# Performance work log

Measured on AMD Instinct MI355X. Metric: run time of the kernel, lower is better.

The kernel has to match this reference:

```python
import jax, jax.numpy as jnp
import numpy as np

B, S, D, H, T = 64, 512, 768, 384, 22  # batch, seq, bert dim, lstm hidden, tagset+2


def setup_inputs() -> dict:
    key = jax.random.key(0)
    ks = jax.random.split(key, 14)
    hidden_states = jax.random.normal(ks[0], (B, S, D), jnp.float32)
    # strictly increasing wordpiece start offsets, -1 padded (per-sample variable length)
    nw = np.array([S // 2 - (b % 16) * 4 for b in range(B)])  # number of valid start ids
    sid = -np.ones((B, S), np.int64)
    msk = np.zeros((B, S), np.int64)
    for b in range(B):
        sid[b, : nw[b]] = 1 + 2 * np.arange(nw[b])  # max = 2*nw-1 <= S-1
        msk[b, : nw[b] + 1] = 1  # word-level mask: nw+1 words incl. CLS slot
    start_ids = jnp.asarray(sid)
    masks = jnp.asarray(msk)
    sc = 0.05
    h0 = jax.random.normal(ks[1], (2, B, H), jnp.float32)
    c0 = jax.random.normal(ks[2], (2, B, H), jnp.float32)
    W_ih_f = jax.random.normal(ks[3], (4 * H, D), jnp.float32) * sc
    W_hh_f = jax.random.normal(ks[4], (4 * H, H), jnp.float32) * sc
    b_ih_f = jax.random.normal(ks[5], (4 * H,), jnp.float32) * sc
    b_hh_f = jax.random.normal(ks[6], (4 * H,), jnp.float32) * sc
    W_ih_b = jax.random.normal(ks[7], (4 * H, D), jnp.float32) * sc
    W_hh_b = jax.random.normal(ks[8], (4 * H, H), jnp.float32) * sc
    b_ih_b = jax.random.normal(ks[9], (4 * H,), jnp.float32) * sc
    b_hh_b = jax.random.normal(ks[10], (4 * H,), jnp.float32) * sc
    W_lin = jax.random.normal(ks[11], (T, 2 * H), jnp.float32) * sc
    b_lin = jax.random.normal(ks[12], (T,), jnp.float32) * sc
    return {"hidden_states": hidden_states, "h0": h0, "c0": c0,
            "W_ih_f": W_ih_f, "W_hh_f": W_hh_f, "b_ih_f": b_ih_f, "b_hh_f": b_hh_f,
            "W_ih_b": W_ih_b, "W_hh_b": W_hh_b, "b_ih_b": b_ih_b, "b_hh_b": b_hh_b,
            "W_lin": W_lin, "b_lin": b_lin, "start_ids": start_ids, "masks": masks}


def _lstm_dir(x, h0, c0, Wih, Whh, bih, bhh, reverse):
    # x: [B,S,D]; torch gate order i,f,g,o
    xg = jnp.einsum('bsd,gd->bsg', x, Wih) + bih + bhh  # [B,S,4H]
    xs = jnp.swapaxes(xg, 0, 1)  # [S,B,4H]
    if reverse:
        xs = xs[::-1]

    def step(carry, xt):
        h, c = carry
        g = xt + h @ Whh.T
        i, f, gg, o = jnp.split(g, 4, axis=-1)
        c = jax.nn.sigmoid(f) * c + jax.nn.sigmoid(i) * jnp.tanh(gg)
        h = jax.nn.sigmoid(o) * jnp.tanh(c)
        return (h, c), h

    _, hs = jax.lax.scan(step, (h0, c0), xs)
    if reverse:
        hs = hs[::-1]
    return jnp.swapaxes(hs, 0, 1)  # [B,S,H]


def _align(hidden_states, start_ids, masks):
    # word t embedding: t==0 -> token 0 (CLS); 1<=t<n -> token start_ids[t]-1
    # (last wordpiece of word t); t==n -> token start_ids[n-1]; else zero-pad.
    Bb, Ss, _ = hidden_states.shape
    t = jnp.arange(Ss)[None, :]
    valid = start_ids >= 0
    n = valid.sum(-1)  # [B] number of valid start ids
    last_sid = jnp.take_along_axis(start_ids, (n - 1)[:, None], axis=1)  # [B,1]
    idx = jnp.where(t == 0, 0,
          jnp.where(t < n[:, None], start_ids - 1,
          jnp.where(t == n[:, None], last_sid, 0)))
    idx = jnp.clip(idx, 0, Ss - 1)
    gathered = jnp.take_along_axis(hidden_states, idx[:, :, None], axis=1)
    sent_len = masks.sum(-1)  # word-level lengths (second loop in torch code)
    keep = (t < sent_len[:, None])[:, :, None]
    return jnp.where(keep, gathered, 0.0)


def reference(hidden_states, h0, c0, W_ih_f, W_hh_f, b_ih_f, b_hh_f,
              W_ih_b, W_hh_b, b_ih_b, b_hh_b, W_lin, b_lin, start_ids, masks):
    embeds = _align(hidden_states, start_ids, masks)  # q=1,k=0 => wordpiece-only
    hf = _lstm_dir(embeds, h0[0], c0[0], W_ih_f, W_hh_f, b_ih_f, b_hh_f, False)
    hb = _lstm_dir(embeds, h0[1], c0[1], W_ih_b, W_hh_b, b_ih_b, b_hh_b, True)
    lstm_out = jnp.concatenate([hf, hb], axis=-1)  # [B,S,2H]
    # dropout1 is identity in eval mode
    feats = lstm_out @ W_lin.T + b_lin  # [B,S,T]
    return feats
```

## Files before the change

kernel.cpp:

```cpp
#include <hip/hip_runtime.h>

typedef unsigned short u16;
typedef unsigned int u32;
typedef unsigned long long u64;

typedef short bf16x8 __attribute__((ext_vector_type(8)));
typedef float f32x4 __attribute__((ext_vector_type(4)));
typedef u32 u32x4 __attribute__((ext_vector_type(4)));

#define NB 64
#define NS 512
#define ND 768
#define NH 384
#define NT_OUT 22
#define S2 272
#define NG 1536
#define MGEMM (NB*S2)
#define MAGIC 0x5A5AA5A5u
#define MAX_RETRY 1000000

__device__ __forceinline__ u16 f2b(float f) {
    u32 u = __float_as_uint(f);
    u32 r = (u + 0x7fffu + ((u >> 16) & 1u)) >> 16;
    return (u16)r;
}
__device__ __forceinline__ float b2f(u16 s) { return __uint_as_float(((u32)s) << 16); }

__device__ __forceinline__ float sigm(float x) {
    return __builtin_amdgcn_rcpf(1.f + __expf(-x));
}
__device__ __forceinline__ float tanh_(float x) {
    return 1.f - 2.f * __builtin_amdgcn_rcpf(1.f + __expf(2.f * x));
}

__device__ __forceinline__ void gl_lds16(const void* g, void* l) {
    __builtin_amdgcn_global_load_lds(
        (const __attribute__((address_space(1))) unsigned int*)g,
        (__attribute__((address_space(3))) unsigned int*)l, 16, 0, 0);
}

__device__ __forceinline__ u32 ld_sc0(const int* p) {
    u32 v;
    asm volatile("global_load_dword %0, %1, off sc0 nt\n\t"
                 "s_waitcnt vmcnt(0)"
                 : "=&v"(v) : "v"(p) : "memory");
    return v;
}
__device__ __forceinline__ void st_sc0(int* p, u32 v) {
    asm volatile("global_store_dword %0, %1, off sc0" :: "v"(p), "v"(v) : "memory");
}

__device__ __forceinline__ void ld6_fast_nw(const u32* p,
        u32x4& A, u32x4& B, u32x4& C, u32x4& D, u32x4& E, u32x4& F) {
    asm volatile(
        "global_load_dwordx4 %0, %6, off sc0 nt\n\t"
        "global_load_dwordx4 %1, %6, off offset:16 sc0 nt\n\t"
        "global_load_dwordx4 %2, %6, off offset:128 sc0 nt\n\t"
        "global_load_dwordx4 %3, %6, off offset:144 sc0 nt\n\t"
        "global_load_dwordx4 %4, %6, off offset:256 sc0 nt\n\t"
        "global_load_dwordx4 %5, %6, off offset:272 sc0 nt"
        : "=&v"(A), "=&v"(B), "=&v"(C), "=&v"(D), "=&v"(E), "=&v"(F)
        : "v"(p) : "memory");
}
__device__ __forceinline__ void ld6_fast_wt(const u32* p,
        u32x4& A, u32x4& B, u32x4& C, u32x4& D, u32x4& E, u32x4& F) {
    asm volatile(
        "global_load_dwordx4 %0, %6, off sc0 nt\n\t"
        "global_load_dwordx4 %1, %6, off offset:16 sc0 nt\n\t"
        "global_load_dwordx4 %2, %6, off offset:128 sc0 nt\n\t"
        "global_load_dwordx4 %3, %6, off offset:144 sc0 nt\n\t"
        "global_load_dwordx4 %4, %6, off offset:256 sc0 nt\n\t"
        "global_load_dwordx4 %5, %6, off offset:272 sc0 nt\n\t"
        "s_waitcnt vmcnt(0)"
        : "=&v"(A), "=&v"(B), "=&v"(C), "=&v"(D), "=&v"(E), "=&v"(F)
        : "v"(p) : "memory");
}
__device__ __forceinline__ void ld6_slow(const u32* p,
        u32x4& A, u32x4& B, u32x4& C, u32x4& D, u32x4& E, u32x4& F) {
    #pragma unroll
    for (int e = 0; e < 4; e++) {
        A[e] = __hip_atomic_load(p + e,      __ATOMIC_RELAXED, __HIP_MEMORY_SCOPE_AGENT);
        B[e] = __hip_atomic_load(p + 4 + e,  __ATOMIC_RELAXED, __HIP_MEMORY_SCOPE_AGENT);
        C[e] = __hip_atomic_load(p + 32 + e, __ATOMIC_RELAXED, __HIP_MEMORY_SCOPE_AGENT);
        D[e] = __hip_atomic_load(p + 36 + e, __ATOMIC_RELAXED, __HIP_MEMORY_SCOPE_AGENT);
        E[e] = __hip_atomic_load(p + 64 + e, __ATOMIC_RELAXED, __HIP_MEMORY_SCOPE_AGENT);
        F[e] = __hip_atomic_load(p + 68 + e, __ATOMIC_RELAXED, __HIP_MEMORY_SCOPE_AGENT);
    }
}
__device__ __forceinline__ void ld6_nw(bool fast, const u32* p,
        u32x4& A, u32x4& B, u32x4& C, u32x4& D, u32x4& E, u32x4& F) {
    if (fast) ld6_fast_nw(p, A, B, C, D, E, F);
    else      ld6_slow(p, A, B, C, D, E, F);
}
__device__ __forceinline__ void ld6_wt(bool fast, const u32* p,
        u32x4& A, u32x4& B, u32x4& C, u32x4& D, u32x4& E, u32x4& F) {
    if (fast) ld6_fast_wt(p, A, B, C, D, E, F);
    else      ld6_slow(p, A, B, C, D, E, F);
}
__device__ __forceinline__ void st8(bool fast, u32* p, u32x4 lo, u32x4 hi) {
    if (fast)
        asm volatile("global_store_dwordx4 %0, %1, off sc0\n\t"
                     "global_store_dwordx4 %0, %2, off offset:16 sc0"
                     :: "v"(p), "v"(lo), "v"(hi) : "memory");
    else {
        #pragma unroll
        for (int e = 0; e < 4; e++) {
            __hip_atomic_store(p + e,     lo[e], __ATOMIC_RELAXED, __HIP_MEMORY_SCOPE_AGENT);
            __hip_atomic_store(p + 4 + e, hi[e], __ATOMIC_RELAXED, __HIP_MEMORY_SCOPE_AGENT);
        }
    }
}
#define WAIT_VM(N) do { __builtin_amdgcn_sched_barrier(0); \
    asm volatile("s_waitcnt vmcnt(" #N ")" ::: "memory"); \
    __builtin_amdgcn_sched_barrier(0); } while (0)
__device__ __forceinline__ void ldsbar() {
    asm volatile("s_waitcnt lgkmcnt(0)" ::: "memory");
    __builtin_amdgcn_s_barrier();
    __builtin_amdgcn_sched_barrier(0);
}

__device__ __forceinline__ u32 sum6(const u32x4& a, const u32x4& b, const u32x4& c,
                                    const u32x4& d, const u32x4& e, const u32x4& f) {
    u32 s = (a[0] & 0xffffu) + (a[1] & 0xffffu) + (a[2] & 0xffffu) + (a[3] & 0xffffu);
    s += (b[0] & 0xffffu) + (b[1] & 0xffffu) + (b[2] & 0xffffu) + (b[3] & 0xffffu);
    s += (c[0] & 0xffffu) + (c[1] & 0xffffu) + (c[2] & 0xffffu) + (c[3] & 0xffffu);
    s += (d[0] & 0xffffu) + (d[1] & 0xffffu) + (d[2] & 0xffffu) + (d[3] & 0xffffu);
    s += (e[0] & 0xffffu) + (e[1] & 0xffffu) + (e[2] & 0xffffu) + (e[3] & 0xffffu);
    s += (f[0] & 0xffffu) + (f[1] & 0xffffu) + (f[2] & 0xffffu) + (f[3] & 0xffffu);
    return s;
}
__device__ __forceinline__ bf16x8 packf(const u32x4& lo, const u32x4& hi) {
    union { u32 q[4]; bf16x8 v; } U;
    U.q[0] = __builtin_amdgcn_perm(lo[1], lo[0], 0x07060302u);
    U.q[1] = __builtin_amdgcn_perm(lo[3], lo[2], 0x07060302u);
    U.q[2] = __builtin_amdgcn_perm(hi[1], hi[0], 0x07060302u);
    U.q[3] = __builtin_amdgcn_perm(hi[3], hi[2], 0x07060302u);
    return U.v;
}

__global__ void k_prep(const float* __restrict__ hidden, const int* __restrict__ start_ids,
                       const int* __restrict__ masks, u16* __restrict__ embeds) {
    int b = blockIdx.x >> 2;
    int quarter = blockIdx.x & 3;
    int tid = threadIdx.x;
    __shared__ int red[256];
    int cn = 0, cm = 0;
    for (int s = tid; s < NS; s += 256) {
        cn += (start_ids[b * NS + s] >= 0) ? 1 : 0;
        cm += (masks[b * NS + s] != 0) ? 1 : 0;
    }
    red[tid] = cn + (cm << 16);
    __syncthreads();
    #pragma unroll
    for (int off = 128; off > 0; off >>= 1) {
        if (tid < off) red[tid] += red[tid + off];
        __syncthreads();
    }
    int n = red[0] & 0xffff;
    int slen = red[0] >> 16;
    n = min(max(n, 1), NS);
    int last = start_ids[b * NS + n - 1];
    for (int t = quarter * 68; t < quarter * 68 + 68; ++t) {
        int idx;
        if (t == 0) idx = 0;
        else if (t < n) idx = start_ids[b * NS + t] - 1;
        else if (t == n) idx = last;
        else idx = 0;
        idx = min(max(idx, 0), NS - 1);
        bool keep = t < slen;
        const float* src = hidden + ((size_t)b * NS + idx) * ND;
        u16* dst = embeds + ((size_t)b * S2 + t) * ND;
        if (tid < 192) {
            float4 v = keep ? *(const float4*)(src + tid * 4) : make_float4(0.f, 0.f, 0.f, 0.f);
            union { u16 u[4]; uint2 q; } pk;
            pk.u[0] = f2b(v.x); pk.u[1] = f2b(v.y); pk.u[2] = f2b(v.z); pk.u[3] = f2b(v.w);
            *(uint2*)(dst + tid * 4) = pk.q;
        }
    }
}

__global__ void k_weights(const float* __restrict__ wf, const float* __restrict__ wb,
                          const float* __restrict__ bihf, const float* __restrict__ bhhf,
                          const float* __restrict__ bihb, const float* __restrict__ bhhb,
                          const float* __restrict__ h0,
                          u16* __restrict__ wihcat, float* __restrict__ biascat,
                          u16* __restrict__ h0buf) {
    int i0 = blockIdx.x * blockDim.x + threadIdx.x;
    int NTH = gridDim.x * blockDim.x;
    for (size_t i = i0; i < (size_t)2 * NG * ND; i += NTH) {
        size_t nrow = i / ND, k = i - nrow * ND;
        float v = (nrow < NG) ? wf[nrow * ND + k] : wb[(nrow - NG) * ND + k];
        wihcat[i] = f2b(v);
    }
    for (int i = i0; i < 2 * NG; i += NTH)
        biascat[i] = (i < NG) ? bihf[i] + bhhf[i] : bihb[i - NG] + bhhb[i - NG];
    for (int i = i0; i < 2 * NB * NH; i += NTH) h0buf[i] = f2b(h0[i]);
}

__global__ void k_packwhh(const float* __restrict__ whhf, const float* __restrict__ whhb,
                          u16* __restrict__ pack) {
    int ft = blockIdx.x * 256 + threadIdx.x;
    if (ft >= 2 * 4 * 4 * 6 * 12 * 64) return;
    int lane = ft & 63;
    int grp = ft >> 6;
    int ks = grp % 12; grp /= 12;
    int nt = grp % 6;  grp /= 6;
    int w  = grp & 3;  grp >>= 2;
    int qc = grp & 3;
    int d  = grp >> 2;
    const float* W = d ? whhb : whhf;
    int col = w * NH + qc * 96 + nt * 16 + (lane & 15);
    int k0 = ks * 32 + (lane >> 4) * 8;
    u16* dst = pack + (size_t)ft * 8;
    #pragma unroll
    for (int e = 0; e < 8; e++) dst[e] = f2b(W[(size_t)col * NH + k0 + e]);
}

__launch_bounds__(256, 2)
__global__ void k_gemm(const u16* __restrict__ A, const u16* __restrict__ Bw,
                       const float* __restrict__ biascat, u16* __restrict__ xg) {
    __shared__ u16 As[128 * 32];
    __shared__ u16 Bs[128 * 32];
    int tid = threadIdx.x;
    int lane = tid & 63, wid = tid >> 6;
    int l15 = lane & 15, q4 = lane >> 4;
    int bn = blockIdx.x;
    int bm = blockIdx.y;
    int wm = (wid >> 1) * 64, wn = (wid & 1) * 64;
    f32x4 acc[4][4] = {};
    for (int k0 = 0; k0 < ND; k0 += 32) {
        #pragma unroll
        for (int j = 0; j < 2; j++) {
            int fl = tid + j * 256;
            int row = fl >> 2, cb = fl & 3;
            const u16* ga = A + (size_t)(bm * 128 + row) * ND + k0 + cb * 8;
            gl_lds16(ga, &As[(size_t)(wid * 64 + j * 256) * 8]);
            const u16* gb = Bw + (size_t)(bn * 128 + row) * ND + k0 + cb * 8;
            gl_lds16(gb, &Bs[(size_t)(wid * 64 + j * 256) * 8]);
        }
        __syncthreads();
        bf16x8 af[4], bf[4];
        #pragma unroll
        for (int mt = 0; mt < 4; mt++)
            af[mt] = *(const bf16x8*)&As[(wm + mt * 16 + l15) * 32 + q4 * 8];
        #pragma unroll
        for (int nt = 0; nt < 4; nt++)
            bf[nt] = *(const bf16x8*)&Bs[(wn + nt * 16 + l15) * 32 + q4 * 8];
        #pragma unroll
        for (int mt = 0; mt < 4; mt++)
            #pragma unroll
            for (int nt = 0; nt < 4; nt++)
                acc[mt][nt] = __builtin_amdgcn_mfma_f32_16x16x32_bf16(af[mt], bf[nt], acc[mt][nt], 0, 0, 0);
        __syncthreads();
    }
    #pragma unroll
    for (int nt = 0; nt < 4; nt++) {
        int gn = bn * 128 + wn + nt * 16 + l15;
        int d = gn >= NG ? 1 : 0;
        int col = gn - d * NG;
        float bias = biascat[gn];
        #pragma unroll
        for (int mt = 0; mt < 4; mt++) {
            #pragma unroll
            for (int r = 0; r < 4; r++) {
                int m = bm * 128 + wm + mt * 16 + q4 * 4 + r;
                int b = m / S2, t = m - b * S2;
                float v = acc[mt][nt][r] + bias;
                xg[((size_t)(d * NB + b) * S2 + t) * NG + col] = f2b(v);
            }
        }
    }
}

__launch_bounds__(256, 1)
__global__ void k_recur(const u16* __restrict__ whhpack, const u16* __restrict__ xg,
                        const float* __restrict__ biascat, const u16* __restrict__ h0buf,
                        const float* __restrict__ c0, u16* __restrict__ hout,
                        int* __restrict__ flags, u32* __restrict__ xch) {
    const int blk = blockIdx.x;
    const int qc = blk >> 3;
    const int cl = blk & 7;
    const int d = cl >> 2;
    const int g = cl & 3;
    const int tid = threadIdx.x, lane = tid & 63, w = tid >> 6;
    const int q4 = lane >> 4, l15 = lane & 15;

    __shared__ float preact[4][16 * 100];
    __shared__ u16 hlds[16 * 104];
    __shared__ int s_fast;

    bf16x8 bfr[6][12];
    #pragma unroll
    for (int nt = 0; nt < 6; nt++)
        #pragma unroll
        for (int j = 0; j < 12; j++) {
            int ksg = ((qc + (j / 3)) & 3) * 3 + (j % 3);
            bfr[nt][j] = *(const bf16x8*)(whhpack +
                ((size_t)((((d * 4 + qc) * 4 + w) * 6 + nt) * 12 + ksg) * 64 + lane) * 8);
        }

    const int bb = tid / 12;
    const int j0 = (tid % 12) * 8;
    float cre[8];
    if (tid < 192) {
        const float* cp = c0 + (size_t)(d * NB + g * 16 + bb) * NH + qc * 96 + j0;
        #pragma unroll
        for (int e = 0; e < 8; e++) cre[e] = cp[e];
    }
    float biasreg[6];
    #pragma unroll
    for (int nt = 0; nt < 6; nt++)
        biasreg[nt] = biascat[d * NG + w * NH + qc * 96 + nt * 16 + l15];

    if (tid == 0) {
        int* pzb = flags + cl * 64;
        int* pmb = flags + 2048 + cl * 64;
        st_sc0(pzb + qc * 16, MAGIC);
        u32 seen = 1u << qc;
        for (int spin = 0; spin < 512 && seen != 0xFu; ++spin) {
            #pragma unroll
            for (int r = 0; r < 4; ++r)
                if (!((seen >> r) & 1u) && ld_sc0(pzb + r * 16) == MAGIC) seen |= 1u << r;
            __builtin_amdgcn_s_sleep(2);
        }
        __hip_atomic_store(pmb + qc * 16, (int)(0x100u | seen),
                           __ATOMIC_RELAXED, __HIP_MEMORY_SCOPE_AGENT);
        u32 m = 0xFu;
        int spin2 = 0;
        #pragma unroll
        for (int r = 0; r < 4; ++r) {
            u32 v;
            do {
                v = (u32)__hip_atomic_load(pmb + r * 16, __ATOMIC_RELAXED,
                                           __HIP_MEMORY_SCOPE_AGENT);
            } while (!(v & 0x100u) && ++spin2 < MAX_RETRY);
            m &= v;
        }
        s_fast = ((m & 0xFu) == 0xFu && spin2 < MAX_RETRY) ? 1 : 0;
    }
    __syncthreads();
    const bool fast = (s_fast != 0);

    const u16* xgd = xg + (size_t)d * NB * S2 * NG;

    u32 cr[6][4];
    auto issue_preload = [&](int it2) -> bool {
        int s2 = d ? (NS - 1 - it2) : it2;
        bool ok = (s2 >= 0) && (s2 < S2);
        int s2c = min(max(s2, 0), S2 - 1);
        const u16* rp = xgd + ((size_t)(g * 16) * S2 + s2c) * NG + w * NH + qc * 96 + l15;
        #pragma unroll
        for (int r = 0; r < 4; r++) {
            const u16* base = rp + (size_t)(q4 * 4 + r) * S2 * NG;
            asm volatile(
                "global_load_ushort %0, %6, off\n\t"
                "global_load_ushort %1, %6, off offset:32\n\t"
                "global_load_ushort %2, %6, off offset:64\n\t"
                "global_load_ushort %3, %6, off offset:96\n\t"
                "global_load_ushort %4, %6, off offset:128\n\t"
                "global_load_ushort %5, %6, off offset:160"
                : "=&v"(cr[0][r]), "=&v"(cr[1][r]), "=&v"(cr[2][r]),
                  "=&v"(cr[3][r]), "=&v"(cr[4][r]), "=&v"(cr[5][r])
                : "v"(base) : "memory");
        }
        return ok;
    };
    bool vld = issue_preload(0);

    #pragma unroll 1
    for (int it = 0; it < NS; ++it) {
        int s = d ? (NS - 1 - it) : it;
        f32x4 acc[6];

        if (it == 0) {
            WAIT_VM(0);
            #pragma unroll
            for (int nt = 0; nt < 6; nt++)
                #pragma unroll
                for (int r = 0; r < 4; r++)
                    acc[nt][r] = vld ? __uint_as_float(cr[nt][r] << 16) : biasreg[nt];
            vld = issue_preload(1);
            const u16* hp = h0buf + (size_t)(d * NB + g * 16) * NH;
            #pragma unroll
            for (int j = 0; j < 12; j++) {
                int ksg = ((qc + (j / 3)) & 3) * 3 + (j % 3);
                bf16x8 af = *(const bf16x8*)(hp + (size_t)l15 * NH + ksg * 32 + q4 * 8);
                #pragma unroll
                for (int nt = 0; nt < 6; nt++)
                    acc[nt] = __builtin_amdgcn_mfma_f32_16x16x32_bf16(af, bfr[nt][j], acc[nt], 0, 0, 0);
            }
        } else {
            const u32 T = (u32)it;
            const u32 want = T * 24u;
            u32* xrow = xch + (((size_t)(T & 3u) * 8 + cl) * 16 + l15) * 384 + q4 * 8;
            u32* pA = xrow + ((qc + 1) & 3) * 96;
            u32* pB = xrow + ((qc + 2) & 3) * 96;
            u32* pC = xrow + ((qc + 3) & 3) * 96;
            u32x4 a0, a1, a2, a3, a4, a5, b0, b1, b2, b3, b4, b5, e0, e1, e2, e3, e4, e5;
            ld6_nw(fast, pA, a0, a1, a2, a3, a4, a5);
            ld6_nw(fast, pB, b0, b1, b2, b3, b4, b5);
            ld6_nw(fast, pC, e0, e1, e2, e3, e4, e5);
            WAIT_VM(18);
            #pragma unroll
            for (int nt = 0; nt < 6; nt++)
                #pragma unroll
                for (int r = 0; r < 4; r++)
                    acc[nt][r] = vld ? __uint_as_float(cr[nt][r] << 16) : biasreg[nt];
            vld = issue_preload(it + 1);
            bf16x8 afo0 = *(const bf16x8*)&hlds[l15 * 104 + 0 * 32 + q4 * 8];
            bf16x8 afo1 = *(const bf16x8*)&hlds[l15 * 104 + 1 * 32 + q4 * 8];
            bf16x8 afo2 = *(const bf16x8*)&hlds[l15 * 104 + 2 * 32 + q4 * 8];
            #pragma unroll
            for (int nt = 0; nt < 6; nt++)
                acc[nt] = __builtin_amdgcn_mfma_f32_16x16x32_bf16(afo0, bfr[nt][0], acc[nt], 0, 0, 0);
            #pragma unroll
            for (int nt = 0; nt < 6; nt++)
                acc[nt] = __builtin_amdgcn_mfma_f32_16x16x32_bf16(afo1, bfr[nt][1], acc[nt], 0, 0, 0);
            #pragma unroll
            for (int nt = 0; nt < 6; nt++)
                acc[nt] = __builtin_amdgcn_mfma_f32_16x16x32_bf16(afo2, bfr[nt][2], acc[nt], 0, 0, 0);
            int tries;
            WAIT_VM(36);
            tries = 0;
            while (!__all(sum6(a0, a1, a2, a3, a4, a5) == want) && ++tries < MAX_RETRY)
                ld6_wt(fast, pA, a0, a1, a2, a3, a4, a5);
            {
                bf16x8 fA0 = packf(a0, a1), fA1 = packf(a2, a3), fA2 = packf(a4, a5);
                #pragma unroll
                for (int nt = 0; nt < 6; nt++)
                    acc[nt] = __builtin_amdgcn_mfma_f32_16x16x32_bf16(fA0, bfr[nt][3], acc[nt], 0, 0, 0);
                #pragma unroll
                for (int nt = 0; nt < 6; nt++)
                    acc[nt] = __builtin_amdgcn_mfma_f32_16x16x32_bf16(fA1, bfr[nt][4], acc[nt], 0, 0, 0);
                #pragma unroll
                for (int nt = 0; nt < 6; nt++)
                    acc[nt] = __builtin_amdgcn_mfma_f32_16x16x32_bf16(fA2, bfr[nt][5], acc[nt], 0, 0, 0);
            }
            WAIT_VM(30);
            tries = 0;
            while (!__all(sum6(b0, b1, b2, b3, b4, b5) == want) && ++tries < MAX_RETRY)
                ld6_wt(fast, pB, b0, b1, b2, b3, b4, b5);
            {
                bf16x8 fB0 = packf(b0, b1), fB1 = packf(b2, b3), fB2 = packf(b4, b5);
                #pragma unroll
                for (int nt = 0; nt < 6; nt++)
                    acc[nt] = __builtin_amdgcn_mfma_f32_16x16x32_bf16(fB0, bfr[nt][6], acc[nt], 0, 0, 0);
                #pragma unroll
                for (int nt = 0; nt < 6; nt++)
                    acc[nt] = __builtin_amdgcn_mfma_f32_16x16x32_bf16(fB1, bfr[nt][7], acc[nt], 0, 0, 0);
                #pragma unroll
                for (int nt = 0; nt < 6; nt++)
                    acc[nt] = __builtin_amdgcn_mfma_f32_16x16x32_bf16(fB2, bfr[nt][8], acc[nt], 0, 0, 0);
            }
            WAIT_VM(24);
            tries = 0;
            while (!__all(sum6(e0, e1, e2, e3, e4, e5) == want) && ++tries < MAX_RETRY)
                ld6_wt(fast, pC, e0, e1, e2, e3, e4, e5);
            {
                bf16x8 fC0 = packf(e0, e1), fC1 = packf(e2, e3), fC2 = packf(e4, e5);
                #pragma unroll
                for (int nt = 0; nt < 6; nt++)
                    acc[nt] = __builtin_amdgcn_mfma_f32_16x16x32_bf16(fC0, bfr[nt][9], acc[nt], 0, 0, 0);
                #pragma unroll
                for (int nt = 0; nt < 6; nt++)
                    acc[nt] = __builtin_amdgcn_mfma_f32_16x16x32_bf16(fC1, bfr[nt][10], acc[nt], 0, 0, 0);
                #pragma unroll
                for (int nt = 0; nt < 6; nt++)
                    acc[nt] = __builtin_amdgcn_mfma_f32_16x16x32_bf16(fC2, bfr[nt][11], acc[nt], 0, 0, 0);
            }
        }

        #pragma unroll
        for (int nt = 0; nt < 6; nt++)
            #pragma unroll
            for (int r = 0; r < 4; r++)
                preact[w][(q4 * 4 + r) * 100 + nt * 16 + l15] = acc[nt][r];
        ldsbar();

        if (tid < 192) {
            int idx = bb * 100 + j0;
            u16* ho = hout + (((size_t)(d * NB + g * 16 + bb)) * NS + s) * NH + qc * 96 + j0;
            union { u16 u[8]; u32x4 v4; } pk;
            #pragma unroll
            for (int e = 0; e < 8; e++) {
                float gi = preact[0][idx + e], gf = preact[1][idx + e];
                float gg = preact[2][idx + e], go = preact[3][idx + e];
                float c = cre[e];
                float cn = sigm(gf) * c + sigm(gi) * tanh_(gg);
                float hn = sigm(go) * tanh_(cn);
                cre[e] = cn;
                pk.u[e] = f2b(hn);
            }
            u32 t2 = (u32)it + 1u;
            u32x4 lo, hi;
            lo[0] = ((u32)pk.u[0] << 16) | t2; lo[1] = ((u32)pk.u[1] << 16) | t2;
            lo[2] = ((u32)pk.u[2] << 16) | t2; lo[3] = ((u32)pk.u[3] << 16) | t2;
            hi[0] = ((u32)pk.u[4] << 16) | t2; hi[1] = ((u32)pk.u[5] << 16) | t2;
            hi[2] = ((u32)pk.u[6] << 16) | t2; hi[3] = ((u32)pk.u[7] << 16) | t2;
            u32* xp = xch + (((size_t)(t2 & 3u) * 8 + cl) * 16 + bb) * 384 + qc * 96 + j0;
            st8(fast, xp, lo, hi);
            *(u32x4*)ho = pk.v4;
            *(u32x4*)&hlds[bb * 104 + j0] = pk.v4;
        }
        ldsbar();
    }
}

__global__ void k_final(const u16* __restrict__ hout, const float* __restrict__ wlin,
                        const float* __restrict__ blin, float* __restrict__ out) {
    int r = blockIdx.x * 256 + threadIdx.x;
    int b = r >> 9, t = r & 511;
    const u16* hf = hout + ((size_t)b * NS + t) * NH;
    const u16* hb = hout + ((size_t)(NB + b) * NS + t) * NH;
    float acc[NT_OUT];
    #pragma unroll
    for (int tt = 0; tt < NT_OUT; tt++) acc[tt] = blin[tt];
    #pragma unroll 1
    for (int half = 0; half < 2; half++) {
        const u16* hp = half ? hb : hf;
        #pragma unroll 1
        for (int k8 = 0; k8 < NH / 8; k8++) {
            uint4 pk = *(const uint4*)(hp + k8 * 8);
            float x[8];
            x[0] = __uint_as_float(pk.x << 16); x[1] = __uint_as_float(pk.x & 0xffff0000u);
            x[2] = __uint_as_float(pk.y << 16); x[3] = __uint_as_float(pk.y & 0xffff0000u);
            x[4] = __uint_as_float(pk.z << 16); x[5] = __uint_as_float(pk.z & 0xffff0000u);
            x[6] = __uint_as_float(pk.w << 16); x[7] = __uint_as_float(pk.w & 0xffff0000u);
            int kk = half * NH + k8 * 8;
            #pragma unroll
            for (int e = 0; e < 8; e++)
                #pragma unroll
                for (int tt = 0; tt < NT_OUT; tt++)
                    acc[tt] += x[e] * wlin[tt * (2 * NH) + kk + e];
        }
    }
    float* op = out + (size_t)r * NT_OUT;
    #pragma unroll
    for (int tt = 0; tt < NT_OUT; tt++) op[tt] = acc[tt];
}

extern "C" void kernel_launch(void* const* d_in, const int* in_sizes, int n_in,
                              void* d_out, int out_size, void* d_ws, size_t ws_size,
                              hipStream_t stream) {
    const float* hidden = (const float*)d_in[0];
    const float* h0     = (const float*)d_in[1];
    const float* c0     = (const float*)d_in[2];
    const float* Wihf   = (const float*)d_in[3];
    const float* Whhf   = (const float*)d_in[4];
    const float* bihf   = (const float*)d_in[5];
    const float* bhhf   = (const float*)d_in[6];
    const float* Wihb   = (const float*)d_in[7];
    const float* Whhb   = (const float*)d_in[8];
    const float* bihb   = (const float*)d_in[9];
    const float* bhhb   = (const float*)d_in[10];
    const float* Wlin   = (const float*)d_in[11];
    const float* blin   = (const float*)d_in[12];
    const int* start_ids = (const int*)d_in[13];
    const int* masks     = (const int*)d_in[14];
    float* out = (float*)d_out;

    char* ws = (char*)d_ws;
    size_t off = 0;
    auto alloc = [&](size_t bytes) { void* p = ws + off; off += (bytes + 255) & ~(size_t)255; return p; };
    u16* embeds   = (u16*)alloc((size_t)MGEMM * ND * 2);
    u16* wihcat   = (u16*)alloc((size_t)2 * NG * ND * 2);
    float* biascat = (float*)alloc((size_t)2 * NG * 4);
    u16* whhpack  = (u16*)alloc((size_t)2 * NG * NH * 2);
    u16* h0buf    = (u16*)alloc((size_t)2 * NB * NH * 2);
    u16* xg       = (u16*)alloc((size_t)2 * NB * S2 * NG * 2);
    u16* hout     = (u16*)alloc((size_t)2 * NB * NS * NH * 2);
    int* flags    = (int*)alloc((size_t)8 * NS * 4);
    u32* xch      = (u32*)alloc((size_t)4 * 8 * 16 * 384 * 4);

    (void)hipMemsetAsync(flags, 0, (size_t)8 * NS * 4, stream);
    (void)hipMemsetAsync(xch, 0, (size_t)4 * 8 * 16 * 384 * 4, stream);
    k_prep<<<256, 256, 0, stream>>>(hidden, start_ids, masks, embeds);
    k_weights<<<512, 256, 0, stream>>>(Wihf, Wihb, bihf, bhhf, bihb, bhhb, h0,
                                       wihcat, biascat, h0buf);
    k_packwhh<<<576, 256, 0, stream>>>(Whhf, Whhb, whhpack);
    dim3 ggrid(2 * NG / 128, MGEMM / 128);
    k_gemm<<<ggrid, 256, 0, stream>>>(embeds, wihcat, biascat, xg);
    k_recur<<<32, 256, 0, stream>>>(whhpack, xg, biascat, h0buf, c0, hout, flags, xch);
    k_final<<<128, 256, 0, stream>>>(hout, Wlin, blin, out);
}
```

Measured before the change: 2.895 ms.

## Spread LSTM cell update over all 256 threads and defer preload issue

The elementwise LSTM cell update previously ran on 192 of 256 threads with 8 elements each. It now runs on all 256 threads with 6 elements each, using dwordx2 exchange stores and 32-bit hout/LDS stores. This shortens the serial gate-update phase on the recurrent critical path. The preload of the next step's input projections is moved after the exchange polling, so the vmcnt waits only track exchange loads and fewer outstanding loads compete early. In exchange it issues more, smaller stores and gives the preload less time to overlap.

Result: faster. 2.729 ms (-5.7%).

```diff
diff --git a/kernel.cpp b/kernel.cpp
--- a/kernel.cpp
+++ b/kernel.cpp
@@ -7,6 +7,7 @@
 typedef short bf16x8 __attribute__((ext_vector_type(8)));
 typedef float f32x4 __attribute__((ext_vector_type(4)));
 typedef u32 u32x4 __attribute__((ext_vector_type(4)));
+typedef u32 u32x2 __attribute__((ext_vector_type(2)));
 
 #define NB 64
 #define NS 512
@@ -96,19 +97,6 @@
         u32x4& A, u32x4& B, u32x4& C, u32x4& D, u32x4& E, u32x4& F) {
     if (fast) ld6_fast_wt(p, A, B, C, D, E, F);
     else      ld6_slow(p, A, B, C, D, E, F);
-}
-__device__ __forceinline__ void st8(bool fast, u32* p, u32x4 lo, u32x4 hi) {
-    if (fast)
-        asm volatile("global_store_dwordx4 %0, %1, off sc0\n\t"
-                     "global_store_dwordx4 %0, %2, off offset:16 sc0"
-                     :: "v"(p), "v"(lo), "v"(hi) : "memory");
-    else {
-        #pragma unroll
-        for (int e = 0; e < 4; e++) {
-            __hip_atomic_store(p + e,     lo[e], __ATOMIC_RELAXED, __HIP_MEMORY_SCOPE_AGENT);
-            __hip_atomic_store(p + 4 + e, hi[e], __ATOMIC_RELAXED, __HIP_MEMORY_SCOPE_AGENT);
-        }
-    }
 }
 #define WAIT_VM(N) do { __builtin_amdgcn_sched_barrier(0); \
     asm volatile("s_waitcnt vmcnt(" #N ")" ::: "memory"); \
@@ -299,13 +287,13 @@
                 ((size_t)((((d * 4 + qc) * 4 + w) * 6 + nt) * 12 + ksg) * 64 + lane) * 8);
         }
 
-    const int bb = tid / 12;
-    const int j0 = (tid % 12) * 8;
-    float cre[8];
-    if (tid < 192) {
-        const float* cp = c0 + (size_t)(d * NB + g * 16 + bb) * NH + qc * 96 + j0;
-        #pragma unroll
-        for (int e = 0; e < 8; e++) cre[e] = cp[e];
+    const int bb = tid >> 4;
+    const int jo = (tid & 15) * 6;
+    float cre[6];
+    {
+        const float* cp = c0 + (size_t)(d * NB + g * 16 + bb) * NH + qc * 96 + jo;
+        #pragma unroll
+        for (int e = 0; e < 6; e++) cre[e] = cp[e];
     }
     float biasreg[6];
     #pragma unroll
@@ -406,7 +394,6 @@
                 #pragma unroll
                 for (int r = 0; r < 4; r++)
                     acc[nt][r] = vld ? __uint_as_float(cr[nt][r] << 16) : biasreg[nt];
-            vld = issue_preload(it + 1);
             bf16x8 afo0 = *(const bf16x8*)&hlds[l15 * 104 + 0 * 32 + q4 * 8];
             bf16x8 afo1 = *(const bf16x8*)&hlds[l15 * 104 + 1 * 32 + q4 * 8];
             bf16x8 afo2 = *(const bf16x8*)&hlds[l15 * 104 + 2 * 32 + q4 * 8];
@@ -420,7 +407,7 @@
             for (int nt = 0; nt < 6; nt++)
                 acc[nt] = __builtin_amdgcn_mfma_f32_16x16x32_bf16(afo2, bfr[nt][2], acc[nt], 0, 0, 0);
             int tries;
-            WAIT_VM(36);
+            WAIT_VM(12);
             tries = 0;
             while (!__all(sum6(a0, a1, a2, a3, a4, a5) == want) && ++tries < MAX_RETRY)
                 ld6_wt(fast, pA, a0, a1, a2, a3, a4, a5);
@@ -436,7 +423,7 @@
                 for (int nt = 0; nt < 6; nt++)
                     acc[nt] = __builtin_amdgcn_mfma_f32_16x16x32_bf16(fA2, bfr[nt][5], acc[nt], 0, 0, 0);
             }
-            WAIT_VM(30);
+            WAIT_VM(6);
             tries = 0;
             while (!__all(sum6(b0, b1, b2, b3, b4, b5) == want) && ++tries < MAX_RETRY)
                 ld6_wt(fast, pB, b0, b1, b2, b3, b4, b5);
@@ -452,10 +439,11 @@
                 for (int nt = 0; nt < 6; nt++)
                     acc[nt] = __builtin_amdgcn_mfma_f32_16x16x32_bf16(fB2, bfr[nt][8], acc[nt], 0, 0, 0);
             }
-            WAIT_VM(24);
+            WAIT_VM(0);
             tries = 0;
             while (!__all(sum6(e0, e1, e2, e3, e4, e5) == want) && ++tries < MAX_RETRY)
                 ld6_wt(fast, pC, e0, e1, e2, e3, e4, e5);
+            vld = issue_preload(it + 1);
             {
                 bf16x8 fC0 = packf(e0, e1), fC1 = packf(e2, e3), fC2 = packf(e4, e5);
                 #pragma unroll
@@ -477,12 +465,13 @@
                 preact[w][(q4 * 4 + r) * 100 + nt * 16 + l15] = acc[nt][r];
         ldsbar();
 
-        if (tid < 192) {
-            int idx = bb * 100 + j0;
-            u16* ho = hout + (((size_t)(d * NB + g * 16 + bb)) * NS + s) * NH + qc * 96 + j0;
-            union { u16 u[8]; u32x4 v4; } pk;
-            #pragma unroll
-            for (int e = 0; e < 8; e++) {
+        {
+            int idx = bb * 100 + jo;
+            u16* ho = hout + (((size_t)(d * NB + g * 16 + bb)) * NS + s) * NH + qc * 96 + jo;
+            union { u16 u[6]; u32 d3[3]; } pk;
+            u32 t2 = (u32)it + 1u;
+            #pragma unroll
+            for (int e = 0; e < 6; e++) {
                 float gi = preact[0][idx + e], gf = preact[1][idx + e];
                 float gg = preact[2][idx + e], go = preact[3][idx + e];
                 float c = cre[e];
@@ -491,16 +480,32 @@
                 cre[e] = cn;
                 pk.u[e] = f2b(hn);
             }
-            u32 t2 = (u32)it + 1u;
-            u32x4 lo, hi;
-            lo[0] = ((u32)pk.u[0] << 16) | t2; lo[1] = ((u32)pk.u[1] << 16) | t2;
-            lo[2] = ((u32)pk.u[2] << 16) | t2; lo[3] = ((u32)pk.u[3] << 16) | t2;
-            hi[0] = ((u32)pk.u[4] << 16) | t2; hi[1] = ((u32)pk.u[5] << 16) | t2;
-            hi[2] = ((u32)pk.u[6] << 16) | t2; hi[3] = ((u32)pk.u[7] << 16) | t2;
-            u32* xp = xch + (((size_t)(t2 & 3u) * 8 + cl) * 16 + bb) * 384 + qc * 96 + j0;
-            st8(fast, xp, lo, hi);
-            *(u32x4*)ho = pk.v4;
-            *(u32x4*)&hlds[bb * 104 + j0] = pk.v4;
+            u32x2 s0, s1, s2;
+            s0[0] = ((u32)pk.u[0] << 16) | t2; s0[1] = ((u32)pk.u[1] << 16) | t2;
+            s1[0] = ((u32)pk.u[2] << 16) | t2; s1[1] = ((u32)pk.u[3] << 16) | t2;
+            s2[0] = ((u32)pk.u[4] << 16) | t2; s2[1] = ((u32)pk.u[5] << 16) | t2;
+            u32* xp = xch + (((size_t)(t2 & 3u) * 8 + cl) * 16 + bb) * 384 + qc * 96 + jo;
+            if (fast)
+                asm volatile(
+                    "global_store_dwordx2 %0, %1, off sc0\n\t"
+                    "global_store_dwordx2 %0, %2, off offset:8 sc0\n\t"
+                    "global_store_dwordx2 %0, %3, off offset:16 sc0"
+                    :: "v"(xp), "v"(s0), "v"(s1), "v"(s2) : "memory");
+            else {
+                __hip_atomic_store(xp,     s0[0], __ATOMIC_RELAXED, __HIP_MEMORY_SCOPE_AGENT);
+                __hip_atomic_store(xp + 1, s0[1], __ATOMIC_RELAXED, __HIP_MEMORY_SCOPE_AGENT);
+                __hip_atomic_store(xp + 2, s1[0], __ATOMIC_RELAXED, __HIP_MEMORY_SCOPE_AGENT);
+                __hip_atomic_store(xp + 3, s1[1], __ATOMIC_RELAXED, __HIP_MEMORY_SCOPE_AGENT);
+                __hip_atomic_store(xp + 4, s2[0], __ATOMIC_RELAXED, __HIP_MEMORY_SCOPE_AGENT);
+                __hip_atomic_store(xp + 5, s2[1], __ATOMIC_RELAXED, __HIP_MEMORY_SCOPE_AGENT);
+            }
+            *(u32*)(ho)     = pk.d3[0];
+            *(u32*)(ho + 2) = pk.d3[1];
+            *(u32*)(ho + 4) = pk.d3[2];
+            u16* hl = &hlds[bb * 104 + jo];
+            *(u32*)(hl)     = pk.d3[0];
+            *(u32*)(hl + 2) = pk.d3[1];
+            *(u32*)(hl + 4) = pk.d3[2];
         }
         ldsbar();
     }
```
